# Performance work log

Measured on AMD Instinct MI355X. Metric: run time of the kernel, lower is better.

## Reference

```python
import jax, jax.numpy as jnp
import numpy as np
from jax import lax

L, E, H, V, T = 4096, 512, 512, 50000, 32
START, END = 0, 1
NEG = -10000.0


def setup_inputs() -> dict:
    key = jax.random.key(0)
    ks = jax.random.split(key, 16)
    s = 0.1  # keep activations in a sane range
    inp = {
        'sentence': jax.random.randint(ks[0], (L,), 0, V, dtype=jnp.int32),
        'embed':  jax.random.normal(ks[1], (V, E)) * s,
        'w_ih_f': jax.random.normal(ks[2], (4 * H, E)) * s,
        'w_hh_f': jax.random.normal(ks[3], (4 * H, H)) * s,
        'b_ih_f': jax.random.normal(ks[4], (4 * H,)) * s,
        'b_hh_f': jax.random.normal(ks[5], (4 * H,)) * s,
        'w_ih_b': jax.random.normal(ks[6], (4 * H, E)) * s,
        'w_hh_b': jax.random.normal(ks[7], (4 * H, H)) * s,
        'b_ih_b': jax.random.normal(ks[8], (4 * H,)) * s,
        'b_hh_b': jax.random.normal(ks[9], (4 * H,)) * s,
        'w_out':  jax.random.normal(ks[10], (T, 2 * H)) * s,
        'b_out':  jax.random.normal(ks[11], (T,)) * s,
        'h0':     jax.random.normal(ks[13], (2, H)),
        'c0':     jax.random.normal(ks[14], (2, H)),
    }
    trans = jax.random.normal(ks[12], (T, T))
    # CRF constraints: never transition into START, never leave from END
    trans = trans.at[START, :].set(NEG).at[:, END].set(NEG)
    inp['trans'] = trans
    return inp


def _lstm_dir(xs, w_ih, w_hh, b_ih, b_hh, h0, c0, reverse):
    # xs: (L, E). PyTorch gate order: i, f, g, o. Precompute input projection.
    x_proj = xs @ w_ih.T + (b_ih + b_hh)  # (L, 4H)

    def step(carry, xp):
        h, c = carry
        gates = xp + h @ w_hh.T
        i, f, g, o = jnp.split(gates, 4)
        i, f, o = jax.nn.sigmoid(i), jax.nn.sigmoid(f), jax.nn.sigmoid(o)
        g = jnp.tanh(g)
        c = f * c + i * g
        h = o * jnp.tanh(c)
        return (h, c), h

    _, hs = lax.scan(step, (h0, c0), x_proj, reverse=reverse)
    return hs  # (L, H)


def reference(sentence, embed, w_ih_f, w_hh_f, b_ih_f, b_hh_f,
              w_ih_b, w_hh_b, b_ih_b, b_hh_b, w_out, b_out, trans, h0, c0):
    xs = embed[sentence]  # (L, E)
    hs_f = _lstm_dir(xs, w_ih_f, w_hh_f, b_ih_f, b_hh_f, h0[0], c0[0], False)
    hs_b = _lstm_dir(xs, w_ih_b, w_hh_b, b_ih_b, b_hh_b, h0[1], c0[1], True)
    feats = jnp.concatenate([hs_f, hs_b], axis=1) @ w_out.T + b_out  # (L, T)

    # Viterbi forward: trans[next, prev]
    init_v = jnp.full((T,), NEG).at[START].set(0.0)

    def vstep(fv, feat):
        scores = trans + fv[None, :]          # (T_next, T_prev)
        bptr = jnp.argmax(scores, axis=1)     # (T,)
        fv_new = jnp.max(scores, axis=1) + feat
        return fv_new, bptr

    fv, bptrs = lax.scan(vstep, init_v, feats)  # bptrs: (L, T)
    terminal = fv + trans[END]
    score = jnp.max(terminal)
    last_tag = jnp.argmax(terminal)

    # Backtrace (reverse scan): path[L-1]=last_tag, path[i]=bptrs[i+1][path[i+1]]
    def back(tag, bp):
        return bp[tag], tag

    _, path = lax.scan(back, last_tag, bptrs, reverse=True)  # (L,)
    return score, path
```

## Files before the change

### kernel.cpp

```cpp
#include <hip/hip_runtime.h>
#include <stdint.h>

#define L_SEQ 4096
#define E_DIM 512
#define H_DIM 512
#define G_DIM 2048
#define NTAG  32

typedef unsigned long long u64;
typedef unsigned short     u16;
typedef unsigned char      u8;

__device__ __forceinline__ float bf2f(u16 u) {
    union { unsigned int i; float f; } v; v.i = ((unsigned int)u) << 16; return v.f;
}
__device__ __forceinline__ bool sniff_f32(const void* trans_raw) {
    const u16* p = (const u16*)trans_raw;
    return p[0] != p[1];
}
__device__ __forceinline__ float ldf(const void* base, long idx, bool isf32) {
    if (isf32) return ((const float*)base)[idx];
    return bf2f(((const u16*)base)[idx]);
}
__device__ __forceinline__ void unpack8_bf16(const u16* src, float* dst) {
    uint4 p = *(const uint4*)src;
    dst[0] = __uint_as_float(p.x << 16); dst[1] = __uint_as_float(p.x & 0xffff0000u);
    dst[2] = __uint_as_float(p.y << 16); dst[3] = __uint_as_float(p.y & 0xffff0000u);
    dst[4] = __uint_as_float(p.z << 16); dst[5] = __uint_as_float(p.z & 0xffff0000u);
    dst[6] = __uint_as_float(p.w << 16); dst[7] = __uint_as_float(p.w & 0xffff0000u);
}

#define LOG2E 1.44269504088896340736f
__device__ __forceinline__ float fsig(float x) {
    return __builtin_amdgcn_rcpf(1.f + __builtin_amdgcn_exp2f(-x * LOG2E));
}
__device__ __forceinline__ float ftanh(float x) {
    return 1.f - 2.f * __builtin_amdgcn_rcpf(1.f + __builtin_amdgcn_exp2f(x * (2.f * LOG2E)));
}

__global__ __launch_bounds__(256) void k_xproj(
    const int* __restrict__ sent, const void* __restrict__ embed,
    const void* __restrict__ w_ih_f, const void* __restrict__ b_ih_f, const void* __restrict__ b_hh_f,
    const void* __restrict__ w_ih_b, const void* __restrict__ b_ih_b, const void* __restrict__ b_hh_b,
    const void* __restrict__ trans_raw,
    float* __restrict__ xp_f, float* __restrict__ xp_b)
{
    const bool isf32 = sniff_f32(trans_raw);
    const int dir = (int)blockIdx.y;
    const void* W  = dir ? w_ih_b : w_ih_f;
    const void* bi = dir ? b_ih_b : b_ih_f;
    const void* bh = dir ? b_hh_b : b_hh_f;
    float* xp = dir ? xp_b : xp_f;
    const int m0 = (int)blockIdx.x * 16;
    const int tid = (int)threadIdx.x;

    __shared__ float xs[16][520];
    __shared__ float wl[16][520];

    {
        const int r = tid >> 4, c0 = (tid & 15) * 32;
        const long row = sent[m0 + r];
        if (isf32) {
            const float* src = (const float*)embed + row * E_DIM + c0;
            #pragma unroll
            for (int i = 0; i < 32; i += 4) *(float4*)&xs[r][c0 + i] = *(const float4*)(src + i);
        } else {
            const u16* src = (const u16*)embed + row * E_DIM + c0;
            #pragma unroll
            for (int i = 0; i < 32; i += 8) unpack8_bf16(src + i, &xs[r][c0 + i]);
        }
    }
    __syncthreads();

    const int mi = tid >> 4, gi = tid & 15;
    for (int gb = 0; gb < 128; ++gb) {
        const int g0 = gb * 16;
        {
            const int r = tid >> 4, c0 = (tid & 15) * 32;
            if (isf32) {
                const float* src = (const float*)W + (long)(g0 + r) * E_DIM + c0;
                #pragma unroll
                for (int i = 0; i < 32; i += 4) *(float4*)&wl[r][c0 + i] = *(const float4*)(src + i);
            } else {
                const u16* src = (const u16*)W + (long)(g0 + r) * E_DIM + c0;
                #pragma unroll
                for (int i = 0; i < 32; i += 8) unpack8_bf16(src + i, &wl[r][c0 + i]);
            }
        }
        __syncthreads();

        float acc = 0.f;
        #pragma unroll 4
        for (int k = 0; k < E_DIM; k += 4) {
            const float4 xv = *(const float4*)&xs[mi][k];
            const float4 wv = *(const float4*)&wl[gi][k];
            acc = fmaf(xv.x, wv.x, acc); acc = fmaf(xv.y, wv.y, acc);
            acc = fmaf(xv.z, wv.z, acc); acc = fmaf(xv.w, wv.w, acc);
        }
        const int g = g0 + gi;
        const float bias = ldf(bi, g, isf32) + ldf(bh, g, isf32);
        xp[(long)(m0 + mi) * G_DIM + g] = acc + bias;
        __syncthreads();
    }
}

__global__ __launch_bounds__(256, 1) void k_lstm(
    const void* __restrict__ w_hh_f, const void* __restrict__ w_hh_b,
    const void* __restrict__ h0, const void* __restrict__ c0,
    const void* __restrict__ trans_raw,
    const float* __restrict__ xp_f, const float* __restrict__ xp_b,
    u64* __restrict__ hsT_f, u64* __restrict__ hsT_b)
{
    const bool isf32 = sniff_f32(trans_raw);
    const int dir = (int)(blockIdx.x >> 5);
    const int wg  = (int)(blockIdx.x & 31);
    const int j0  = wg * 16;
    const void* Whh = dir ? w_hh_b : w_hh_f;
    const float* xp = dir ? xp_b : xp_f;
    u64* hsT        = dir ? hsT_b : hsT_f;

    const int tid = (int)threadIdx.x;
    const int rp  = tid >> 3;
    const int ks  = tid & 7;
    const int d   = rp >> 1;
    const int gp  = rp & 1;
    const int g0r = gp * 2;

    __shared__ float h_lds[512 + 32];

    float wreg[2][64];
    #pragma unroll
    for (int rl = 0; rl < 2; ++rl) {
        const long roff = (long)((g0r + rl) * H_DIM + j0 + d) * H_DIM + ks * 64;
        if (isf32) {
            const float* wrow = (const float*)Whh + roff;
            #pragma unroll
            for (int b = 0; b < 16; ++b) *(float4*)&wreg[rl][b * 4] = *(const float4*)(wrow + b * 4);
        } else {
            const u16* wrow = (const u16*)Whh + roff;
            #pragma unroll
            for (int b = 0; b < 8; ++b) unpack8_bf16(wrow + b * 8, &wreg[rl][b * 8]);
        }
    }

    {
        const int w0 = tid * 2;
        h_lds[w0 + ((w0 >> 6) << 2)]     = ldf(h0, dir * H_DIM + w0, isf32);
        h_lds[w0 + 1 + ((w0 >> 6) << 2)] = ldf(h0, dir * H_DIM + w0 + 1, isf32);
    }

    const bool is_act = ((tid & 15) == 0);
    const int  jown   = j0 + d;
    float cst = 0.f;
    if (is_act) cst = ldf(c0, dir * H_DIM + jown, isf32);

    const int b16 = tid >> 4, off = tid & 15;
    const int pidx = is_act ? -1 : (b16 * 15 + off - 1);
    int jw0 = 0, jw1 = 0, jw2 = -1;
    if (pidx >= 0) {
        const int w0 = 2 * pidx, w1 = 2 * pidx + 1;
        jw0 = w0 + (w0 >= j0 ? 16 : 0);
        jw1 = w1 + (w1 >= j0 ? 16 : 0);
        if (pidx < 16) { const int w2 = 480 + pidx; jw2 = w2 + (w2 >= j0 ? 16 : 0); }
    }

    int t = dir ? (L_SEQ - 1) : 0;
    float xc0 = 0, xc1 = 0, xc2 = 0, xc3 = 0, xn0 = 0, xn1 = 0, xn2 = 0, xn3 = 0;
    if (is_act) {
        const float* xr = xp + (long)t * G_DIM + jown;
        xn0 = xr[0]; xn1 = xr[H_DIM]; xn2 = xr[2 * H_DIM]; xn3 = xr[3 * H_DIM];
    }
    __syncthreads();

    #pragma unroll 1
    for (int k = 0; k < L_SEQ; ++k) {
        t = dir ? (L_SEQ - 1 - k) : k;
        if (is_act) {
            xc0 = xn0; xc1 = xn1; xc2 = xn2; xc3 = xn3;
            if (k + 1 < L_SEQ) {
                const int nt = dir ? (t - 1) : (t + 1);
                const float* xr = xp + (long)nt * G_DIM + jown;
                xn0 = xr[0]; xn1 = xr[H_DIM]; xn2 = xr[2 * H_DIM]; xn3 = xr[3 * H_DIM];
            }
        }

        float a0 = 0, a1 = 0;
        const float4* hb = (const float4*)(h_lds + ks * 68);
        #pragma unroll
        for (int q = 0; q < 16; ++q) {
            const float4 hv = hb[q];
            a0 = fmaf(wreg[0][4*q+0], hv.x, a0); a0 = fmaf(wreg[0][4*q+1], hv.y, a0);
            a0 = fmaf(wreg[0][4*q+2], hv.z, a0); a0 = fmaf(wreg[0][4*q+3], hv.w, a0);
            a1 = fmaf(wreg[1][4*q+0], hv.x, a1); a1 = fmaf(wreg[1][4*q+1], hv.y, a1);
            a1 = fmaf(wreg[1][4*q+2], hv.z, a1); a1 = fmaf(wreg[1][4*q+3], hv.w, a1);
        }
        #pragma unroll
        for (int m = 1; m < 8; m <<= 1) { a0 += __shfl_xor(a0, m); a1 += __shfl_xor(a1, m); }
        const float b0 = __shfl_xor(a0, 8);
        const float b1 = __shfl_xor(a1, 8);

        if (is_act) {
            const float iv = fsig(a0 + xc0);
            const float fo = fsig(a1 + xc1);
            const float gv = ftanh(b0 + xc2);
            const float ov = fsig(b1 + xc3);
            cst = fo * cst + iv * gv;
            const float hv2 = ov * ftanh(cst);
            h_lds[jown + ((jown >> 6) << 2)] = hv2;
            const u64 pk = (((u64)(unsigned)(k + 1)) << 32) | (u64)__float_as_uint(hv2);
            __hip_atomic_store(&hsT[(long)t * H_DIM + jown], pk,
                               __ATOMIC_RELAXED, __HIP_MEMORY_SCOPE_AGENT);
        }

        if (k + 1 < L_SEQ && pidx >= 0) {
            const unsigned tagv = (unsigned)(k + 1);
            u64* pa0 = &hsT[(long)t * H_DIM + jw0];
            u64* pa1 = &hsT[(long)t * H_DIM + jw1];
            u64* pa2 = (jw2 >= 0) ? &hsT[(long)t * H_DIM + jw2] : pa0;
            u64 v0 = 0, v1 = 0, v2 = 0;
            bool q0 = false, q1 = false, q2 = (jw2 < 0);
            do {
                if (!q0) { v0 = __hip_atomic_load(pa0, __ATOMIC_RELAXED, __HIP_MEMORY_SCOPE_AGENT); }
                if (!q1) { v1 = __hip_atomic_load(pa1, __ATOMIC_RELAXED, __HIP_MEMORY_SCOPE_AGENT); }
                if (!q2) { v2 = __hip_atomic_load(pa2, __ATOMIC_RELAXED, __HIP_MEMORY_SCOPE_AGENT); }
                q0 = q0 || ((unsigned)(v0 >> 32) == tagv);
                q1 = q1 || ((unsigned)(v1 >> 32) == tagv);
                q2 = q2 || ((unsigned)(v2 >> 32) == tagv);
            } while (!(q0 && q1 && q2));
            h_lds[jw0 + ((jw0 >> 6) << 2)] = __uint_as_float((unsigned)v0);
            h_lds[jw1 + ((jw1 >> 6) << 2)] = __uint_as_float((unsigned)v1);
            if (jw2 >= 0) h_lds[jw2 + ((jw2 >> 6) << 2)] = __uint_as_float((unsigned)v2);
        }
        __syncthreads();
    }
}

__global__ __launch_bounds__(256) void k_feats(
    const u64* __restrict__ hsT_f, const u64* __restrict__ hsT_b,
    const void* __restrict__ w_out, const void* __restrict__ b_out,
    const void* __restrict__ trans_raw, float* __restrict__ feats)
{
    const bool isf32 = sniff_f32(trans_raw);
    const int n  = (int)threadIdx.x & 31;
    const int tl = (int)threadIdx.x >> 5;
    const int t  = (int)blockIdx.x * 8 + tl;
    const float* hf  = (const float*)(hsT_f + (long)t * H_DIM);
    const float* hbp = (const float*)(hsT_b + (long)t * H_DIM);
    float acc = ldf(b_out, n, isf32);
    if (isf32) {
        const float* wf = (const float*)w_out + (long)n * 1024;
        const float* wb = wf + 512;
        #pragma unroll 4
        for (int j2 = 0; j2 < 256; ++j2) {
            acc = fmaf(hf [4 * j2],     wf[2 * j2],     acc);
            acc = fmaf(hf [4 * j2 + 2], wf[2 * j2 + 1], acc);
            acc = fmaf(hbp[4 * j2],     wb[2 * j2],     acc);
            acc = fmaf(hbp[4 * j2 + 2], wb[2 * j2 + 1], acc);
        }
    } else {
        const unsigned int* wf = (const unsigned int*)((const u16*)w_out + (long)n * 1024);
        const unsigned int* wb = (const unsigned int*)((const u16*)w_out + (long)n * 1024 + 512);
        #pragma unroll 4
        for (int j2 = 0; j2 < 256; ++j2) {
            const unsigned int wp = wf[j2];
            const unsigned int wq = wb[j2];
            acc = fmaf(hf [4 * j2],     __uint_as_float(wp << 16),         acc);
            acc = fmaf(hf [4 * j2 + 2], __uint_as_float(wp & 0xffff0000u), acc);
            acc = fmaf(hbp[4 * j2],     __uint_as_float(wq << 16),         acc);
            acc = fmaf(hbp[4 * j2 + 2], __uint_as_float(wq & 0xffff0000u), acc);
        }
    }
    feats[(long)t * 32 + n] = acc;
}

__global__ __launch_bounds__(64) void k_viterbi(
    const float* __restrict__ feats, const void* __restrict__ trans_raw,
    u8* __restrict__ bptr, float* __restrict__ out)
{
    const bool isf32 = sniff_f32(trans_raw);
    const int lane = (int)threadIdx.x;
    const int n = lane & 31, half = lane >> 5;
    __shared__ u8 mlds[64 * 32];
    __shared__ u8 entry[64];

    float tr[16];
    #pragma unroll
    for (int i = 0; i < 16; ++i) tr[i] = ldf(trans_raw, n * 32 + half * 16 + i, isf32);
    const float tr_end = ldf(trans_raw, 32 + n, isf32);

    float fvreg = (n == 0) ? 0.f : -10000.f;
    float fnext = feats[n];
    #pragma unroll 1
    for (int tt = 0; tt < L_SEQ; ++tt) {
        const float fcur = fnext;
        const int nt = (tt + 1 < L_SEQ) ? tt + 1 : tt;
        fnext = feats[(long)nt * 32 + n];

        float best = -3.4e38f; int bp = 0;
        #pragma unroll
        for (int i = 0; i < 16; ++i) {
            const float c = tr[i] + __shfl(fvreg, half * 16 + i);
            if (c > best) { best = c; bp = half * 16 + i; }
        }
        const float ob = __shfl_xor(best, 32);
        const int  obp = __shfl_xor(bp, 32);
        if (ob > best || (ob == best && obp < bp)) { best = ob; bp = obp; }

        fvreg = best + fcur;
        if (half == 0) bptr[(long)tt * 32 + n] = (u8)bp;
    }

    float term = (half == 0) ? (fvreg + tr_end) : -3.4e38f;
    int   ti   = (half == 0) ? n : 1000;
    #pragma unroll
    for (int m = 1; m < 64; m <<= 1) {
        const float ov = __shfl_xor(term, m);
        const int   oi = __shfl_xor(ti, m);
        if (ov > term || (ov == term && oi < ti)) { term = ov; ti = oi; }
    }
    if (lane == 0) out[0] = term;
    __syncthreads();

    unsigned cur[32];
    #pragma unroll
    for (int ch = 0; ch < 32; ++ch) cur[ch] = (unsigned)ch;
    const int cbase = lane * 64;
    for (int s = 63; s >= 0; --s) {
        const u8* row = bptr + (long)(cbase + s) * 32;
        #pragma unroll
        for (int ch = 0; ch < 32; ++ch) cur[ch] = row[cur[ch]];
    }
    #pragma unroll
    for (int ch = 0; ch < 32; ++ch) mlds[lane * 32 + ch] = (u8)cur[ch];
    __syncthreads();

    if (lane == 0) {
        int tag = ti;
        for (int c = 63; c >= 0; --c) { entry[c] = (u8)tag; tag = mlds[c * 32 + tag]; }
    }
    __syncthreads();

    {
        int tag = entry[lane];
        for (int s = 63; s >= 0; --s) {
            const int gidx = cbase + s;
            out[1 + gidx] = (float)tag;
            tag = bptr[(long)gidx * 32 + tag];
        }
    }
}

extern "C" void kernel_launch(void* const* d_in, const int* in_sizes, int n_in,
                              void* d_out, int out_size, void* d_ws, size_t ws_size,
                              hipStream_t stream)
{
    (void)in_sizes; (void)n_in; (void)out_size; (void)ws_size;
    const int* sent  = (const int*)d_in[0];
    const void* embed  = d_in[1];
    const void* w_ih_f = d_in[2];
    const void* w_hh_f = d_in[3];
    const void* b_ih_f = d_in[4];
    const void* b_hh_f = d_in[5];
    const void* w_ih_b = d_in[6];
    const void* w_hh_b = d_in[7];
    const void* b_ih_b = d_in[8];
    const void* b_hh_b = d_in[9];
    const void* w_out  = d_in[10];
    const void* b_out  = d_in[11];
    const void* h0     = d_in[12];
    const void* c0     = d_in[13];
    const void* trans  = d_in[14];

    char* ws = (char*)d_ws;
    float* xp_f  = (float*)(ws);
    float* xp_b  = (float*)(ws + (32ull << 20));
    u64*   hsT_f = (u64*)(ws + (64ull << 20));
    u64*   hsT_b = (u64*)(ws + (80ull << 20));
    float* feats = (float*)(ws);
    u8*    bptr  = (u8*)(ws + (1ull << 20));

    k_xproj<<<dim3(256, 2), 256, 0, stream>>>(sent, embed,
        w_ih_f, b_ih_f, b_hh_f, w_ih_b, b_ih_b, b_hh_b, trans, xp_f, xp_b);
    k_lstm<<<64, 256, 0, stream>>>(w_hh_f, w_hh_b, h0, c0, trans, xp_f, xp_b, hsT_f, hsT_b);
    k_feats<<<512, 256, 0, stream>>>(hsT_f, hsT_b, w_out, b_out, trans, feats);
    k_viterbi<<<1, 64, 0, stream>>>(feats, trans, bptr, (float*)d_out);
}
```

Baseline: 12.58 ms.

## Vectorize LSTM cross-block h polling, spread blocks across XCDs, prefetch Viterbi feats

The LSTM kernel now launches 256 blocks and keeps only those with blk&7 < 2, so each direction's 32 workgroups land on a single XCD under round-robin dispatch and share one L2 for the h exchange. The per-step poll for other blocks' hidden values now has fewer threads each issue four 16-byte loads with sc0 inline asm, replacing scalar 64-bit atomic loads. If a bounded spin does not see all tags, a sticky fallback switches to per-element atomic polling. The Viterbi loop is unrolled by four and keeps four feats values in flight instead of one. The inline asm relies on the XCD mapping and on 16-byte loads not tearing with respect to the tag/value pairs.

```diff
diff --git a/kernel.cpp b/kernel.cpp
--- a/kernel.cpp
+++ b/kernel.cpp
@@ -10,6 +10,7 @@
 typedef unsigned long long u64;
 typedef unsigned short     u16;
 typedef unsigned char      u8;
+typedef __attribute__((ext_vector_type(4))) unsigned int uint4v;
 
 __device__ __forceinline__ float bf2f(u16 u) {
     union { unsigned int i; float f; } v; v.i = ((unsigned int)u) << 16; return v.f;
@@ -111,9 +112,11 @@
     const float* __restrict__ xp_f, const float* __restrict__ xp_b,
     u64* __restrict__ hsT_f, u64* __restrict__ hsT_b)
 {
+    const int blk = (int)blockIdx.x;
+    if ((blk & 7) >= 2) return;
     const bool isf32 = sniff_f32(trans_raw);
-    const int dir = (int)(blockIdx.x >> 5);
-    const int wg  = (int)(blockIdx.x & 31);
+    const int dir = blk & 7;
+    const int wg  = blk >> 3;
     const int j0  = wg * 16;
     const void* Whh = dir ? w_hh_b : w_hh_f;
     const float* xp = dir ? xp_b : xp_f;
@@ -154,15 +157,10 @@
     float cst = 0.f;
     if (is_act) cst = ldf(c0, dir * H_DIM + jown, isf32);
 
-    const int b16 = tid >> 4, off = tid & 15;
-    const int pidx = is_act ? -1 : (b16 * 15 + off - 1);
-    int jw0 = 0, jw1 = 0, jw2 = -1;
-    if (pidx >= 0) {
-        const int w0 = 2 * pidx, w1 = 2 * pidx + 1;
-        jw0 = w0 + (w0 >= j0 ? 16 : 0);
-        jw1 = w1 + (w1 >= j0 ? 16 : 0);
-        if (pidx < 16) { const int w2 = 480 + pidx; jw2 = w2 + (w2 >= j0 ? 16 : 0); }
-    }
+    const int c = ((tid & 3) == 1) ? (tid >> 2) : -1;
+    int jw = -1;
+    if (c >= 0 && c < 62) { const int w = c * 8; jw = w + (w >= j0 ? 16 : 0); }
+    int fastmode = 1;
 
     int t = dir ? (L_SEQ - 1) : 0;
     float xc0 = 0, xc1 = 0, xc2 = 0, xc3 = 0, xn0 = 0, xn1 = 0, xn2 = 0, xn3 = 0;
@@ -212,24 +210,55 @@
                                __ATOMIC_RELAXED, __HIP_MEMORY_SCOPE_AGENT);
         }
 
-        if (k + 1 < L_SEQ && pidx >= 0) {
+        if (k + 1 < L_SEQ && jw >= 0) {
             const unsigned tagv = (unsigned)(k + 1);
-            u64* pa0 = &hsT[(long)t * H_DIM + jw0];
-            u64* pa1 = &hsT[(long)t * H_DIM + jw1];
-            u64* pa2 = (jw2 >= 0) ? &hsT[(long)t * H_DIM + jw2] : pa0;
-            u64 v0 = 0, v1 = 0, v2 = 0;
-            bool q0 = false, q1 = false, q2 = (jw2 < 0);
-            do {
-                if (!q0) { v0 = __hip_atomic_load(pa0, __ATOMIC_RELAXED, __HIP_MEMORY_SCOPE_AGENT); }
-                if (!q1) { v1 = __hip_atomic_load(pa1, __ATOMIC_RELAXED, __HIP_MEMORY_SCOPE_AGENT); }
-                if (!q2) { v2 = __hip_atomic_load(pa2, __ATOMIC_RELAXED, __HIP_MEMORY_SCOPE_AGENT); }
-                q0 = q0 || ((unsigned)(v0 >> 32) == tagv);
-                q1 = q1 || ((unsigned)(v1 >> 32) == tagv);
-                q2 = q2 || ((unsigned)(v2 >> 32) == tagv);
-            } while (!(q0 && q1 && q2));
-            h_lds[jw0 + ((jw0 >> 6) << 2)] = __uint_as_float((unsigned)v0);
-            h_lds[jw1 + ((jw1 >> 6) << 2)] = __uint_as_float((unsigned)v1);
-            if (jw2 >= 0) h_lds[jw2 + ((jw2 >> 6) << 2)] = __uint_as_float((unsigned)v2);
+            u64* pw = &hsT[(long)t * H_DIM + jw];
+            uint4v A = {0,0,0,0}, B = {0,0,0,0}, C = {0,0,0,0}, D = {0,0,0,0};
+            bool g0 = false, g1 = false, g2 = false, g3 = false;
+            if (fastmode) {
+                #pragma unroll 1
+                for (int r = 0; r < 64; ++r) {
+                    if (!g0) asm volatile("global_load_dwordx4 %0, %1, off sc0" : "=v"(A) : "v"(pw));
+                    if (!g1) asm volatile("global_load_dwordx4 %0, %1, off sc0" : "=v"(B) : "v"(pw + 2));
+                    if (!g2) asm volatile("global_load_dwordx4 %0, %1, off sc0" : "=v"(C) : "v"(pw + 4));
+                    if (!g3) asm volatile("global_load_dwordx4 %0, %1, off sc0" : "=v"(D) : "v"(pw + 6));
+                    asm volatile("s_waitcnt vmcnt(0)" : "+v"(A), "+v"(B), "+v"(C), "+v"(D));
+                    g0 = g0 || (A.y == tagv && A.w == tagv);
+                    g1 = g1 || (B.y == tagv && B.w == tagv);
+                    g2 = g2 || (C.y == tagv && C.w == tagv);
+                    g3 = g3 || (D.y == tagv && D.w == tagv);
+                    if (g0 && g1 && g2 && g3) break;
+                }
+                if (!(g0 && g1 && g2 && g3)) fastmode = 0;
+            }
+            if (!g0) { u64 v;
+                do { v = __hip_atomic_load(pw + 0, __ATOMIC_RELAXED, __HIP_MEMORY_SCOPE_AGENT); } while ((unsigned)(v >> 32) != tagv);
+                A.x = (unsigned)v;
+                do { v = __hip_atomic_load(pw + 1, __ATOMIC_RELAXED, __HIP_MEMORY_SCOPE_AGENT); } while ((unsigned)(v >> 32) != tagv);
+                A.z = (unsigned)v; }
+            if (!g1) { u64 v;
+                do { v = __hip_atomic_load(pw + 2, __ATOMIC_RELAXED, __HIP_MEMORY_SCOPE_AGENT); } while ((unsigned)(v >> 32) != tagv);
+                B.x = (unsigned)v;
+                do { v = __hip_atomic_load(pw + 3, __ATOMIC_RELAXED, __HIP_MEMORY_SCOPE_AGENT); } while ((unsigned)(v >> 32) != tagv);
+                B.z = (unsigned)v; }
+            if (!g2) { u64 v;
+                do { v = __hip_atomic_load(pw + 4, __ATOMIC_RELAXED, __HIP_MEMORY_SCOPE_AGENT); } while ((unsigned)(v >> 32) != tagv);
+                C.x = (unsigned)v;
+                do { v = __hip_atomic_load(pw + 5, __ATOMIC_RELAXED, __HIP_MEMORY_SCOPE_AGENT); } while ((unsigned)(v >> 32) != tagv);
+                C.z = (unsigned)v; }
+            if (!g3) { u64 v;
+                do { v = __hip_atomic_load(pw + 6, __ATOMIC_RELAXED, __HIP_MEMORY_SCOPE_AGENT); } while ((unsigned)(v >> 32) != tagv);
+                D.x = (unsigned)v;
+                do { v = __hip_atomic_load(pw + 7, __ATOMIC_RELAXED, __HIP_MEMORY_SCOPE_AGENT); } while ((unsigned)(v >> 32) != tagv);
+                D.z = (unsigned)v; }
+            const int d0 = jw + ((jw >> 6) << 2);
+            float4 lo, hi;
+            lo.x = __uint_as_float(A.x); lo.y = __uint_as_float(A.z);
+            lo.z = __uint_as_float(B.x); lo.w = __uint_as_float(B.z);
+            hi.x = __uint_as_float(C.x); hi.y = __uint_as_float(C.z);
+            hi.z = __uint_as_float(D.x); hi.w = __uint_as_float(D.z);
+            *(float4*)&h_lds[d0]     = lo;
+            *(float4*)&h_lds[d0 + 4] = hi;
         }
         __syncthreads();
     }
@@ -289,25 +318,28 @@
     const float tr_end = ldf(trans_raw, 32 + n, isf32);
 
     float fvreg = (n == 0) ? 0.f : -10000.f;
-    float fnext = feats[n];
-    #pragma unroll 1
-    for (int tt = 0; tt < L_SEQ; ++tt) {
-        const float fcur = fnext;
-        const int nt = (tt + 1 < L_SEQ) ? tt + 1 : tt;
-        fnext = feats[(long)nt * 32 + n];
-
+    float f0 = feats[0 * 32 + n], f1 = feats[1 * 32 + n];
+    float f2 = feats[2 * 32 + n], f3 = feats[3 * 32 + n];
+
+    auto step = [&](float& fslot, int ttv) {
+        const float fcur = fslot;
+        if (ttv + 4 < L_SEQ) fslot = feats[(long)(ttv + 4) * 32 + n];
         float best = -3.4e38f; int bp = 0;
         #pragma unroll
         for (int i = 0; i < 16; ++i) {
-            const float c = tr[i] + __shfl(fvreg, half * 16 + i);
-            if (c > best) { best = c; bp = half * 16 + i; }
+            const float cnd = tr[i] + __shfl(fvreg, half * 16 + i);
+            if (cnd > best) { best = cnd; bp = half * 16 + i; }
         }
         const float ob = __shfl_xor(best, 32);
         const int  obp = __shfl_xor(bp, 32);
         if (ob > best || (ob == best && obp < bp)) { best = ob; bp = obp; }
-
         fvreg = best + fcur;
-        if (half == 0) bptr[(long)tt * 32 + n] = (u8)bp;
+        if (half == 0) bptr[(long)ttv * 32 + n] = (u8)bp;
+    };
+
+    #pragma unroll 1
+    for (int tt = 0; tt < L_SEQ; tt += 4) {
+        step(f0, tt); step(f1, tt + 1); step(f2, tt + 2); step(f3, tt + 3);
     }
 
     float term = (half == 0) ? (fvreg + tr_end) : -3.4e38f;
@@ -336,7 +368,7 @@
 
     if (lane == 0) {
         int tag = ti;
-        for (int c = 63; c >= 0; --c) { entry[c] = (u8)tag; tag = mlds[c * 32 + tag]; }
+        for (int cc = 63; cc >= 0; --cc) { entry[cc] = (u8)tag; tag = mlds[cc * 32 + tag]; }
     }
     __syncthreads();
 
@@ -381,7 +413,7 @@
 
     k_xproj<<<dim3(256, 2), 256, 0, stream>>>(sent, embed,
         w_ih_f, b_ih_f, b_hh_f, w_ih_b, b_ih_b, b_hh_b, trans, xp_f, xp_b);
-    k_lstm<<<64, 256, 0, stream>>>(w_hh_f, w_hh_b, h0, c0, trans, xp_f, xp_b, hsT_f, hsT_b);
+    k_lstm<<<256, 256, 0, stream>>>(w_hh_f, w_hh_b, h0, c0, trans, xp_f, xp_b, hsT_f, hsT_b);
     k_feats<<<512, 256, 0, stream>>>(hsT_f, hsT_b, w_out, b_out, trans, feats);
     k_viterbi<<<1, 64, 0, stream>>>(feats, trans, bptr, (float*)d_out);
 }
```

New measurement: 16.54 ms. 31.4% more time.
